# Kernel optimization log

Measured on AMD Instinct MI355X. Metric: run time of the kernel, lower is better.

## Reference

```python
import jax, jax.numpy as jnp
import numpy as np

H = 1024  # hidden_dim
D = 128   # input_dim
B = 128   # batch
S = 512   # seq_len / target_len


def _lstm_cell(inp, h, c, Wih, Whh, bih, bhh):
    # PyTorch gate order: i, f, g, o
    gates = inp @ Wih.T + h @ Whh.T + bih + bhh  # [B, 4H]
    i, f, g, o = jnp.split(gates, 4, axis=-1)
    i = jax.nn.sigmoid(i)
    f = jax.nn.sigmoid(f)
    g = jnp.tanh(g)
    o = jax.nn.sigmoid(o)
    c = f * c + i * g
    h = o * jnp.tanh(c)
    return h, c


def setup_inputs() -> dict:
    key = jax.random.key(0)
    ks = jax.random.split(key, 12)
    k = 1.0 / np.sqrt(H)  # PyTorch LSTM/Linear uniform init bound
    u = lambda kk, shp: jax.random.uniform(kk, shp, jnp.float32, -k, k)
    return {
        "x": jax.random.normal(ks[0], (B, S, D), jnp.float32),
        "enc_Wih": u(ks[1], (4 * H, D)),
        "enc_Whh": u(ks[2], (4 * H, H)),
        "enc_bih": u(ks[3], (4 * H,)),
        "enc_bhh": u(ks[4], (4 * H,)),
        "dec_Wih": u(ks[5], (4 * H, H)),
        "dec_Whh": u(ks[6], (4 * H, H)),
        "dec_bih": u(ks[7], (4 * H,)),
        "dec_bhh": u(ks[8], (4 * H,)),
        "out_W": u(ks[9], (D, H)),
        "out_b": u(ks[10], (D,)),
    }


def reference(x, enc_Wih, enc_Whh, enc_bih, enc_bhh,
              dec_Wih, dec_Whh, dec_bih, dec_bhh, out_W, out_b):
    b, s, _ = x.shape
    h0 = jnp.zeros((b, H), x.dtype)
    c0 = jnp.zeros((b, H), x.dtype)

    # ---- encoder: LSTM over time ----
    def enc_step(carry, xt):
        h, c = carry
        h, c = _lstm_cell(xt, h, c, enc_Wih, enc_Whh, enc_bih, enc_bhh)
        return (h, c), h

    (h_n, c_n), hs = jax.lax.scan(enc_step, (h0, c0), jnp.transpose(x, (1, 0, 2)))
    encoded = jnp.transpose(hs, (1, 0, 2))  # [B, S, H]

    def dec_step(carry, _):
        h, c, inp = carry
        h, c = _lstm_cell(inp, h, c, dec_Wih, dec_Whh, dec_bih, dec_bhh)
        y = h @ out_W.T + out_b  # [B, D]
        return (h, c, y), y

    init = (h_n, c_n, encoded[:, -1, :] @ jnp.eye(H, D, dtype=x.dtype) * 0 + 0)  # placeholder removed below
    # decoder_input starts as last encoder hidden (encoded_seq[:, -1:, :]) but the
    # decoder LSTM input size is H while fed-back outputs have size D in torch code;
    # torch decoder has input_size=hidden_dim, so feeding back D-dim output would
    # error in torch unless D == H. The repo uses it with the first step only having
    # H-dim input; to be runnable and faithful to the intended recurrence we pad the
    # fed-back output to H dims via the same convention torch would require: here we
    # replicate the exact torch graph, which requires feeding H-dim inputs, so we
    # project outputs back implicitly by zero-padding.
    def dec_step_pad(carry, _):
        h, c, inp = carry  # inp: [B, H]
        h, c = _lstm_cell(inp, h, c, dec_Wih, dec_Whh, dec_bih, dec_bhh)
        y = h @ out_W.T + out_b  # [B, D]
        inp_next = jnp.pad(y, ((0, 0), (0, H - D)))
        return (h, c, inp_next), y

    carry0 = (h_n, c_n, encoded[:, -1, :])
    _, ys = jax.lax.scan(dec_step_pad, carry0, None, length=s)
    recon = jnp.transpose(ys, (1, 0, 2))  # [B, S, D]

    recon_loss = jnp.mean(jnp.sum((recon - x) ** 2, axis=(1, 2)))
    return recon, encoded, recon_loss
```

## Files before the change

### kernel.cpp

```cpp
#include <hip/hip_runtime.h>


#define BB 128
#define SS 512
#define DD 128
#define HH 1024
#define G4 4096
#define KENC 1152
#define NBLK 256
#define RP 20
#define SLOTSTRIDE 16

typedef _Float16 half8 __attribute__((ext_vector_type(8)));
typedef float floatx4 __attribute__((ext_vector_type(4)));

__device__ __forceinline__ float sigf(float x) { return 1.0f / (1.0f + __expf(-x)); }
__device__ __forceinline__ float tanhfast(float x) { return 1.0f - 2.0f / (1.0f + __expf(2.0f * x)); }

#define MFMA16(a, b, c) __builtin_amdgcn_mfma_f32_16x16x32_f16((a), (b), (c), 0, 0, 0)

__device__ __forceinline__ half8 ldg_h8_sc(const _Float16* p) {
  floatx4 t;
  asm volatile("global_load_dwordx4 %0, %1, off sc0 sc1" : "=v"(t) : "v"(p) : "memory");
  return __builtin_bit_cast(half8, t);
}
__device__ __forceinline__ void stg_h_sc(_Float16* p, _Float16 v) {
  unsigned u = (unsigned)__builtin_bit_cast(unsigned short, v);
  asm volatile("global_store_short %0, %1, off sc0 sc1" :: "v"(p), "v"(u) : "memory");
}


__global__ void k_prep_encw(const float* __restrict__ eWih, const float* __restrict__ eWhh,
                            _Float16* __restrict__ encW) {
  int r = blockIdx.x;
  for (int k = threadIdx.x; k < KENC; k += blockDim.x) {
    float v = (k < DD) ? eWih[(size_t)r * DD + k] : eWhh[(size_t)r * HH + (k - DD)];
    encW[(size_t)r * KENC + k] = (_Float16)v;
  }
}

__global__ void k_prep_simple(const float* __restrict__ x, const float* __restrict__ dWih,
                              const float* __restrict__ dWhh, const float* __restrict__ oW,
                              const float* __restrict__ eBih, const float* __restrict__ eBhh,
                              const float* __restrict__ dBih, const float* __restrict__ dBhh,
                              const float* __restrict__ oB,
                              _Float16* __restrict__ x16,
                              _Float16* __restrict__ decW1, _Float16* __restrict__ outW16,
                              float* __restrict__ encB, float* __restrict__ decB1,
                              float* __restrict__ decB2,
                              _Float16* __restrict__ hA, float* __restrict__ lossAcc,
                              unsigned* __restrict__ bar) {
  int tid = blockIdx.x * blockDim.x + threadIdx.x;
  int nt = gridDim.x * blockDim.x;
  for (size_t i = tid; i < (size_t)G4 * HH; i += nt)
    decW1[i] = (_Float16)(dWih[i] + dWhh[i]);
  for (size_t i = tid; i < (size_t)BB * SS * DD; i += nt)
    x16[i] = (_Float16)x[i];
  for (size_t i = tid; i < (size_t)DD * HH; i += nt)
    outW16[i] = (_Float16)oW[i];
  for (size_t i = tid; i < (size_t)BB * HH; i += nt)
    hA[i] = (_Float16)0.0f;
  for (size_t i = tid; i < (size_t)NBLK * SLOTSTRIDE; i += nt)
    bar[i] = 0u;
  if (tid == 0) lossAcc[0] = 0.0f;
  if (tid < G4) {
    encB[tid] = eBih[tid] + eBhh[tid];
    float b1 = dBih[tid] + dBhh[tid];
    decB1[tid] = b1;
    float acc = b1;
    for (int j = 0; j < DD; ++j) acc += dWih[(size_t)tid * HH + j] * oB[j];
    decB2[tid] = acc;
  }
}

__global__ void k_prep_decw2(const float* __restrict__ dWih, const float* __restrict__ dWhh,
                             const float* __restrict__ oW, _Float16* __restrict__ decW2) {
  int r = blockIdx.x >> 2;
  int c = ((blockIdx.x & 3) << 8) + threadIdx.x;
  float acc = dWhh[(size_t)r * HH + c];
  for (int j = 0; j < DD; ++j) acc += dWih[(size_t)r * HH + j] * oW[(size_t)j * HH + c];
  decW2[(size_t)r * HH + c] = (_Float16)acc;
}

__device__ __forceinline__ void bar_arrive(unsigned* slot, unsigned step) {
  asm volatile("s_waitcnt vmcnt(0)" ::: "memory");
  __syncthreads();
  if (threadIdx.x == 0)
    __hip_atomic_store(slot, step, __ATOMIC_RELAXED, __HIP_MEMORY_SCOPE_AGENT);
}
__device__ __forceinline__ void bar_wait(unsigned* slots, int polln, unsigned step) {
  int pi = (int)threadIdx.x - (512 - polln);
  if (pi >= 0) {
    unsigned* p = slots + (size_t)pi * SLOTSTRIDE;
    while (__hip_atomic_load(p, __ATOMIC_RELAXED, __HIP_MEMORY_SCOPE_AGENT) < step)
      __builtin_amdgcn_s_sleep(4);
  }
  __syncthreads();
}


__global__ __launch_bounds__(512, 2) void k_seq(
    const float* __restrict__ x, const _Float16* __restrict__ x16,
    const _Float16* __restrict__ encW, const float* __restrict__ encB,
    const _Float16* __restrict__ decW1, const _Float16* __restrict__ decW2,
    const float* __restrict__ decB1, const float* __restrict__ decB2,
    const _Float16* __restrict__ outW, const float* __restrict__ oB,
    _Float16* __restrict__ hA, _Float16* __restrict__ hB,
    float* __restrict__ encOut, float* __restrict__ recon,
    float* __restrict__ lossAcc, float* __restrict__ lossOut,
    unsigned* __restrict__ bar) {
  __shared__ float pl[4][4][2][16][RP];
  __shared__ float red[4][2][16][RP];
  __shared__ float pY[4][2][16][RP];
  __shared__ float redY[2][16][RP];

  const int tid = threadIdx.x;
  const int lane = tid & 63, w = tid >> 6;
  const int n = lane & 15, q = lane >> 4;
  const int ut = (int)blockIdx.x & 63, mtb = (int)blockIdx.x >> 6;
  const int m0 = mtb << 5, u0 = ut << 4;
  const int kh0 = w << 7;

  const int m_l = tid >> 4, u_l = tid & 15;
  const int mtc = m_l >> 4, rowc = m_l & 15;
  const int cm = m0 + m_l, cu = u0 + u_l;
  const size_t hidx = (size_t)cm * HH + cu;

  unsigned* myslot = bar + (size_t)blockIdx.x * SLOTSTRIDE;
  unsigned* grpSlots = bar + (size_t)(mtb * 64) * SLOTSTRIDE;
  float creg = 0.0f;

  half8 bw[4][4];
  half8 xw[4];
  {
    const _Float16* base = encW + (size_t)(u0 + n) * KENC + (size_t)(DD + kh0 + q * 8);
#pragma unroll
    for (int g = 0; g < 4; ++g)
#pragma unroll
      for (int kk = 0; kk < 4; ++kk)
        bw[g][kk] = *(const half8*)(base + (size_t)g * ((size_t)HH * KENC) + kk * 32);
    if (w < 4) {
      const _Float16* xb = encW + (size_t)(u0 + n) * KENC + (size_t)((w << 5) + q * 8);
#pragma unroll
      for (int g = 0; g < 4; ++g)
        xw[g] = *(const half8*)(xb + (size_t)g * ((size_t)HH * KENC));
    }
  }
  float b0 = encB[cu], b1 = encB[HH + cu], b2 = encB[2 * HH + cu], b3 = encB[3 * HH + cu];

  const _Float16* hrowA = hA + (size_t)(m0 + n) * HH + kh0 + q * 8;
  const _Float16* hrowB = hB + (size_t)(m0 + n) * HH + kh0 + q * 8;
  const _Float16* x16r0 = x16 + (size_t)(m0 + n) * ((size_t)SS * DD) + (size_t)((w << 5) + q * 8);
  const _Float16* x16r1 = x16r0 + (size_t)16 * ((size_t)SS * DD);
  float* encPtr = encOut + (size_t)cm * ((size_t)SS * HH) + cu;

  for (int t = 0; t < SS; ++t) {
    floatx4 acc[4][2];
#pragma unroll
    for (int g = 0; g < 4; ++g) {
      acc[g][0] = (floatx4){0, 0, 0, 0};
      acc[g][1] = (floatx4){0, 0, 0, 0};
    }
    if (w < 4) {
      half8 xa0 = *(const half8*)(x16r0 + (size_t)t * DD);
      half8 xa1 = *(const half8*)(x16r1 + (size_t)t * DD);
      acc[0][0] = MFMA16(xa0, xw[0], acc[0][0]); acc[0][1] = MFMA16(xa1, xw[0], acc[0][1]);
      acc[1][0] = MFMA16(xa0, xw[1], acc[1][0]); acc[1][1] = MFMA16(xa1, xw[1], acc[1][1]);
      acc[2][0] = MFMA16(xa0, xw[2], acc[2][0]); acc[2][1] = MFMA16(xa1, xw[2], acc[2][1]);
      acc[3][0] = MFMA16(xa0, xw[3], acc[3][0]); acc[3][1] = MFMA16(xa1, xw[3], acc[3][1]);
    }
    if (t > 0) bar_wait(grpSlots, 64, (unsigned)t);

    const _Float16* h0 = (t & 1) ? hrowB : hrowA;
    const _Float16* h1 = h0 + (size_t)16 * HH;
    half8 ha[4], hb[4];
#pragma unroll
    for (int kk = 0; kk < 4; ++kk) {
      ha[kk] = ldg_h8_sc(h0 + kk * 32);
      hb[kk] = ldg_h8_sc(h1 + kk * 32);
    }
    asm volatile("s_waitcnt vmcnt(0)" ::: "memory");
    __builtin_amdgcn_sched_barrier(0);
#pragma unroll
    for (int kk = 0; kk < 4; ++kk) {
      acc[0][0] = MFMA16(ha[kk], bw[0][kk], acc[0][0]); acc[0][1] = MFMA16(hb[kk], bw[0][kk], acc[0][1]);
      acc[1][0] = MFMA16(ha[kk], bw[1][kk], acc[1][0]); acc[1][1] = MFMA16(hb[kk], bw[1][kk], acc[1][1]);
      acc[2][0] = MFMA16(ha[kk], bw[2][kk], acc[2][0]); acc[2][1] = MFMA16(hb[kk], bw[2][kk], acc[2][1]);
      acc[3][0] = MFMA16(ha[kk], bw[3][kk], acc[3][0]); acc[3][1] = MFMA16(hb[kk], bw[3][kk], acc[3][1]);
    }

    if (w >= 4) {
#pragma unroll
      for (int g = 0; g < 4; ++g)
#pragma unroll
        for (int mt = 0; mt < 2; ++mt)
#pragma unroll
          for (int r = 0; r < 4; ++r)
            pl[w - 4][g][mt][q * 4 + r][n] = acc[g][mt][r];
    }
    __syncthreads();
    if (w < 4) {
#pragma unroll
      for (int g = 0; g < 4; ++g)
#pragma unroll
        for (int mt = 0; mt < 2; ++mt)
#pragma unroll
          for (int r = 0; r < 4; ++r) {
            acc[g][mt][r] += pl[w][g][mt][q * 4 + r][n];
            pl[w][g][mt][q * 4 + r][n] = acc[g][mt][r];
          }
    }
    __syncthreads();
    {
      int base = tid * 4;
      int col = base & 15, row = (base >> 4) & 15, mt = (base >> 8) & 1, g = base >> 9;
      floatx4 s = *(const floatx4*)&pl[0][g][mt][row][col];
      s += *(const floatx4*)&pl[1][g][mt][row][col];
      s += *(const floatx4*)&pl[2][g][mt][row][col];
      s += *(const floatx4*)&pl[3][g][mt][row][col];
      *(floatx4*)&red[g][mt][row][col] = s;
    }
    __syncthreads();
    {
      float gi = sigf(red[0][mtc][rowc][u_l] + b0);
      float gf = sigf(red[1][mtc][rowc][u_l] + b1);
      float gg = tanhfast(red[2][mtc][rowc][u_l] + b2);
      float go = sigf(red[3][mtc][rowc][u_l] + b3);
      float cv = gf * creg + gi * gg;
      creg = cv;
      float hv = go * tanhfast(cv);
      stg_h_sc(((t & 1) ? hA : hB) + hidx, (_Float16)hv);
      encPtr[0] = hv;
      encPtr += HH;
    }
    bar_arrive(myslot, (unsigned)(t + 1));
  }

  {
    const _Float16* base = decW1 + (size_t)(u0 + n) * HH + (size_t)(kh0 + q * 8);
#pragma unroll
    for (int g = 0; g < 4; ++g)
#pragma unroll
      for (int kk = 0; kk < 4; ++kk)
        bw[g][kk] = *(const half8*)(base + (size_t)g * ((size_t)HH * HH) + kk * 32);
  }
  b0 = decB1[cu]; b1 = decB1[HH + cu]; b2 = decB1[2 * HH + cu]; b3 = decB1[3 * HH + cu];

  half8 ow[4];
  if (ut < 8) {
    const _Float16* oro = outW + (size_t)(u0 + n) * HH + (size_t)(kh0 + q * 8);
#pragma unroll
    for (int kk = 0; kk < 4; ++kk) ow[kk] = *(const half8*)(oro + kk * 32);
  }
  const float obv_cu = (ut < 8) ? oB[cu] : 0.0f;

  for (int s = 1; s <= SS; ++s) {
    if (s == 2) {
      const _Float16* base = decW2 + (size_t)(u0 + n) * HH + (size_t)(kh0 + q * 8);
#pragma unroll
      for (int g = 0; g < 4; ++g)
#pragma unroll
        for (int kk = 0; kk < 4; ++kk)
          bw[g][kk] = *(const half8*)(base + (size_t)g * ((size_t)HH * HH) + kk * 32);
      b0 = decB2[cu]; b1 = decB2[HH + cu]; b2 = decB2[2 * HH + cu]; b3 = decB2[3 * HH + cu];
    }
    bar_wait(grpSlots, 64, (unsigned)(511 + s));

    const int p = 511 + s;
    const _Float16* h0 = (p & 1) ? hrowB : hrowA;
    const _Float16* h1 = h0 + (size_t)16 * HH;
    const bool doY = (s >= 2) && (ut < 8);

    floatx4 acc[4][2];
#pragma unroll
    for (int g = 0; g < 4; ++g) {
      acc[g][0] = (floatx4){0, 0, 0, 0};
      acc[g][1] = (floatx4){0, 0, 0, 0};
    }
    floatx4 accY[2];
    accY[0] = (floatx4){0, 0, 0, 0}; accY[1] = (floatx4){0, 0, 0, 0};

    half8 ha[4], hb[4];
#pragma unroll
    for (int kk = 0; kk < 4; ++kk) {
      ha[kk] = ldg_h8_sc(h0 + kk * 32);
      hb[kk] = ldg_h8_sc(h1 + kk * 32);
    }
    asm volatile("s_waitcnt vmcnt(0)" ::: "memory");
    __builtin_amdgcn_sched_barrier(0);
#pragma unroll
    for (int kk = 0; kk < 4; ++kk) {
      acc[0][0] = MFMA16(ha[kk], bw[0][kk], acc[0][0]); acc[0][1] = MFMA16(hb[kk], bw[0][kk], acc[0][1]);
      acc[1][0] = MFMA16(ha[kk], bw[1][kk], acc[1][0]); acc[1][1] = MFMA16(hb[kk], bw[1][kk], acc[1][1]);
      acc[2][0] = MFMA16(ha[kk], bw[2][kk], acc[2][0]); acc[2][1] = MFMA16(hb[kk], bw[2][kk], acc[2][1]);
      acc[3][0] = MFMA16(ha[kk], bw[3][kk], acc[3][0]); acc[3][1] = MFMA16(hb[kk], bw[3][kk], acc[3][1]);
      if (doY) {
        accY[0] = MFMA16(ha[kk], ow[kk], accY[0]);
        accY[1] = MFMA16(hb[kk], ow[kk], accY[1]);
      }
    }

    if (w >= 4) {
#pragma unroll
      for (int g = 0; g < 4; ++g)
#pragma unroll
        for (int mt = 0; mt < 2; ++mt)
#pragma unroll
          for (int r = 0; r < 4; ++r)
            pl[w - 4][g][mt][q * 4 + r][n] = acc[g][mt][r];
      if (doY)
#pragma unroll
        for (int mt = 0; mt < 2; ++mt)
#pragma unroll
          for (int r = 0; r < 4; ++r)
            pY[w - 4][mt][q * 4 + r][n] = accY[mt][r];
    }
    __syncthreads();
    if (w < 4) {
#pragma unroll
      for (int g = 0; g < 4; ++g)
#pragma unroll
        for (int mt = 0; mt < 2; ++mt)
#pragma unroll
          for (int r = 0; r < 4; ++r) {
            acc[g][mt][r] += pl[w][g][mt][q * 4 + r][n];
            pl[w][g][mt][q * 4 + r][n] = acc[g][mt][r];
          }
      if (doY)
#pragma unroll
        for (int mt = 0; mt < 2; ++mt)
#pragma unroll
          for (int r = 0; r < 4; ++r) {
            accY[mt][r] += pY[w][mt][q * 4 + r][n];
            pY[w][mt][q * 4 + r][n] = accY[mt][r];
          }
    }
    __syncthreads();
    {
      int base = tid * 4;
      int col = base & 15, row = (base >> 4) & 15, mt = (base >> 8) & 1, g = base >> 9;
      floatx4 sv = *(const floatx4*)&pl[0][g][mt][row][col];
      sv += *(const floatx4*)&pl[1][g][mt][row][col];
      sv += *(const floatx4*)&pl[2][g][mt][row][col];
      sv += *(const floatx4*)&pl[3][g][mt][row][col];
      *(floatx4*)&red[g][mt][row][col] = sv;
    }
    if (doY && tid < 128) {
      int base = tid * 4;
      int col = base & 15, row = (base >> 4) & 15, mt = (base >> 8) & 1;
      floatx4 sv = *(const floatx4*)&pY[0][mt][row][col];
      sv += *(const floatx4*)&pY[1][mt][row][col];
      sv += *(const floatx4*)&pY[2][mt][row][col];
      sv += *(const floatx4*)&pY[3][mt][row][col];
      *(floatx4*)&redY[mt][row][col] = sv;
    }
    __syncthreads();
    {
      float gi = sigf(red[0][mtc][rowc][u_l] + b0);
      float gf = sigf(red[1][mtc][rowc][u_l] + b1);
      float gg = tanhfast(red[2][mtc][rowc][u_l] + b2);
      float go = sigf(red[3][mtc][rowc][u_l] + b3);
      float cv = gf * creg + gi * gg;
      creg = cv;
      float hv = go * tanhfast(cv);
      stg_h_sc(((p & 1) ? hA : hB) + hidx, (_Float16)hv);
      if (doY) {
        int ty = s - 2;
        float yv = redY[mtc][rowc][u_l] + obv_cu;
        size_t ix = (size_t)cm * ((size_t)SS * DD) + (size_t)ty * DD + cu;
        recon[ix] = yv;
        float e = yv - x[ix];
        float ls = e * e;
#pragma unroll
        for (int off = 32; off; off >>= 1) ls += __shfl_xor(ls, off, 64);
        if (lane == 0) atomicAdd(lossAcc, ls);
      }
    }
    bar_arrive(myslot, (unsigned)(512 + s));
  }

  bar_wait(bar, 256, 1024u);
  if ((int)blockIdx.x < 64 && tid < 64) {
    const int fmt = (int)blockIdx.x >> 3, fdt = (int)blockIdx.x & 7;
    const int fm0 = fmt << 4, d0 = fdt << 4;
    floatx4 a4 = (floatx4){0, 0, 0, 0};
    const _Float16* hrow = hA + (size_t)(fm0 + n) * HH + q * 8;
    const _Float16* orow = outW + (size_t)(d0 + n) * HH + q * 8;
    for (int kb = 0; kb < 32; kb += 8) {
      half8 hh[8];
#pragma unroll
      for (int j = 0; j < 8; ++j) hh[j] = ldg_h8_sc(hrow + (size_t)(kb + j) * 32);
      asm volatile("s_waitcnt vmcnt(0)" ::: "memory");
      __builtin_amdgcn_sched_barrier(0);
#pragma unroll
      for (int j = 0; j < 8; ++j)
        a4 = MFMA16(hh[j], *(const half8*)(orow + (size_t)(kb + j) * 32), a4);
    }
    int d = d0 + n;
    float ob2 = oB[d];
    float ls = 0.0f;
#pragma unroll
    for (int r = 0; r < 4; ++r) {
      int m = fm0 + q * 4 + r;
      float yv = a4[r] + ob2;
      size_t ix = (size_t)m * ((size_t)SS * DD) + (size_t)(SS - 1) * DD + d;
      recon[ix] = yv;
      float e = yv - x[ix];
      ls += e * e;
    }
#pragma unroll
    for (int off = 32; off; off >>= 1) ls += __shfl_xor(ls, off, 64);
    if (lane == 0) atomicAdd(lossAcc, ls);
  }
  bar_arrive(myslot, 1025u);
  bar_wait(bar, 256, 1025u);
  if (blockIdx.x == 0 && tid == 0)
    lossOut[0] = __hip_atomic_load(lossAcc, __ATOMIC_RELAXED, __HIP_MEMORY_SCOPE_AGENT) *
                 (1.0f / (float)BB);
}


extern "C" void kernel_launch(void* const* d_in, const int* in_sizes, int n_in,
                              void* d_out, int out_size, void* d_ws, size_t ws_size,
                              hipStream_t stream) {
  const float* x    = (const float*)d_in[0];
  const float* eWih = (const float*)d_in[1];
  const float* eWhh = (const float*)d_in[2];
  const float* eBih = (const float*)d_in[3];
  const float* eBhh = (const float*)d_in[4];
  const float* dWih = (const float*)d_in[5];
  const float* dWhh = (const float*)d_in[6];
  const float* dBih = (const float*)d_in[7];
  const float* dBhh = (const float*)d_in[8];
  const float* oW   = (const float*)d_in[9];
  const float* oB   = (const float*)d_in[10];

  float* out = (float*)d_out;
  float* recon = out;
  float* encOut = out + (size_t)BB * SS * DD;
  float* lossOut = out + (size_t)BB * SS * DD + (size_t)BB * SS * HH;

  char* p = (char*)d_ws;
  auto alloc = [&](size_t bytes) {
    char* r = p;
    p += (bytes + 255) & ~(size_t)255;
    return r;
  };
  _Float16* encW   = (_Float16*)alloc((size_t)G4 * KENC * 2);
  _Float16* decW1  = (_Float16*)alloc((size_t)G4 * HH * 2);
  _Float16* decW2  = (_Float16*)alloc((size_t)G4 * HH * 2);
  _Float16* outW16 = (_Float16*)alloc((size_t)DD * HH * 2);
  _Float16* x16    = (_Float16*)alloc((size_t)BB * SS * DD * 2);
  float* encB  = (float*)alloc((size_t)G4 * 4);
  float* decB1 = (float*)alloc((size_t)G4 * 4);
  float* decB2 = (float*)alloc((size_t)G4 * 4);
  _Float16* hA = (_Float16*)alloc((size_t)BB * HH * 2);
  _Float16* hB = (_Float16*)alloc((size_t)BB * HH * 2);
  float* lossAcc = (float*)alloc(256);
  unsigned* bar = (unsigned*)alloc((size_t)NBLK * SLOTSTRIDE * 4);
  (void)in_sizes; (void)n_in; (void)out_size; (void)ws_size;

  k_prep_encw<<<G4, 256, 0, stream>>>(eWih, eWhh, encW);
  k_prep_simple<<<2048, 256, 0, stream>>>(x, dWih, dWhh, oW, eBih, eBhh, dBih, dBhh, oB,
                                          x16, decW1, outW16, encB, decB1, decB2, hA,
                                          lossAcc, bar);
  k_prep_decw2<<<G4 * 4, 256, 0, stream>>>(dWih, dWhh, oW, decW2);

  void* args[] = {(void*)&x, (void*)&x16, (void*)&encW, (void*)&encB, (void*)&decW1,
                  (void*)&decW2, (void*)&decB1, (void*)&decB2, (void*)&outW16, (void*)&oB,
                  (void*)&hA, (void*)&hB, (void*)&encOut, (void*)&recon,
                  (void*)&lossAcc, (void*)&lossOut, (void*)&bar};
  (void)hipLaunchCooperativeKernel((void*)k_seq, dim3(NBLK), dim3(512), args, 0, stream);
}
```

Baseline: 6.137 ms.

## Split K per wave with per-wave producer polling and single-pass reduction

Waves are reassigned so each handles one 16-row batch tile and a 256-wide K slice, instead of two row tiles and a 128-wide slice. Each wave now polls only the 16 producer blocks that own its K slice, rather than the whole block waiting on all 64. The two-stage shared-memory reduction with three barriers becomes a single barrier and a direct four-way sum. Loss partials are kept in registers and flushed with one atomic per block at the end, and the poll sleep is shortened. The cost is twice as many weight registers per wave, and the output-projection weights are now reloaded from global memory every step.

New measurement: 5.704 ms. 7.1% less time.

```diff
diff --git a/kernel.cpp b/kernel.cpp
--- a/kernel.cpp
+++ b/kernel.cpp
@@ -82,18 +82,27 @@
   decW2[(size_t)r * HH + c] = (_Float16)acc;
 }
 
-__device__ __forceinline__ void bar_arrive(unsigned* slot, unsigned step) {
+
+__device__ __forceinline__ void block_arrive(unsigned* slot, unsigned step) {
   asm volatile("s_waitcnt vmcnt(0)" ::: "memory");
   __syncthreads();
   if (threadIdx.x == 0)
     __hip_atomic_store(slot, step, __ATOMIC_RELAXED, __HIP_MEMORY_SCOPE_AGENT);
 }
-__device__ __forceinline__ void bar_wait(unsigned* slots, int polln, unsigned step) {
-  int pi = (int)threadIdx.x - (512 - polln);
-  if (pi >= 0) {
-    unsigned* p = slots + (size_t)pi * SLOTSTRIDE;
+__device__ __forceinline__ void wave_wait16(unsigned* slots, unsigned step) {
+  int l = (int)threadIdx.x & 63;
+  if (l < 16) {
+    unsigned* p = slots + (size_t)l * SLOTSTRIDE;
     while (__hip_atomic_load(p, __ATOMIC_RELAXED, __HIP_MEMORY_SCOPE_AGENT) < step)
-      __builtin_amdgcn_s_sleep(4);
+      __builtin_amdgcn_s_sleep(2);
+  }
+}
+__device__ __forceinline__ void bar_wait_all(unsigned* bar, unsigned step) {
+  int pi = (int)threadIdx.x;
+  if (pi < NBLK) {
+    unsigned* p = bar + (size_t)pi * SLOTSTRIDE;
+    while (__hip_atomic_load(p, __ATOMIC_RELAXED, __HIP_MEMORY_SCOPE_AGENT) < step)
+      __builtin_amdgcn_s_sleep(2);
   }
   __syncthreads();
 }
@@ -110,122 +119,88 @@
     float* __restrict__ lossAcc, float* __restrict__ lossOut,
     unsigned* __restrict__ bar) {
   __shared__ float pl[4][4][2][16][RP];
-  __shared__ float red[4][2][16][RP];
   __shared__ float pY[4][2][16][RP];
-  __shared__ float redY[2][16][RP];
+  __shared__ float lred[8];
 
   const int tid = threadIdx.x;
   const int lane = tid & 63, w = tid >> 6;
   const int n = lane & 15, q = lane >> 4;
+  const int mtw = w >> 2, ksl = w & 3;
   const int ut = (int)blockIdx.x & 63, mtb = (int)blockIdx.x >> 6;
   const int m0 = mtb << 5, u0 = ut << 4;
-  const int kh0 = w << 7;
 
   const int m_l = tid >> 4, u_l = tid & 15;
   const int mtc = m_l >> 4, rowc = m_l & 15;
   const int cm = m0 + m_l, cu = u0 + u_l;
   const size_t hidx = (size_t)cm * HH + cu;
 
+  const floatx4 zero4 = {0.0f, 0.0f, 0.0f, 0.0f};
+
   unsigned* myslot = bar + (size_t)blockIdx.x * SLOTSTRIDE;
-  unsigned* grpSlots = bar + (size_t)(mtb * 64) * SLOTSTRIDE;
+  unsigned* prodSlots = bar + (size_t)(mtb * 64 + ksl * 16) * SLOTSTRIDE;
   float creg = 0.0f;
-
-  half8 bw[4][4];
+  float lossReg = 0.0f;
+
+  half8 bw[4][8];
   half8 xw[4];
   {
-    const _Float16* base = encW + (size_t)(u0 + n) * KENC + (size_t)(DD + kh0 + q * 8);
-#pragma unroll
-    for (int g = 0; g < 4; ++g)
-#pragma unroll
-      for (int kk = 0; kk < 4; ++kk)
+    const _Float16* base = encW + (size_t)(u0 + n) * KENC + (size_t)(DD + ksl * 256 + q * 8);
+    const _Float16* xb   = encW + (size_t)(u0 + n) * KENC + (size_t)(ksl * 32 + q * 8);
+#pragma unroll
+    for (int g = 0; g < 4; ++g) {
+#pragma unroll
+      for (int kk = 0; kk < 8; ++kk)
         bw[g][kk] = *(const half8*)(base + (size_t)g * ((size_t)HH * KENC) + kk * 32);
-    if (w < 4) {
-      const _Float16* xb = encW + (size_t)(u0 + n) * KENC + (size_t)((w << 5) + q * 8);
-#pragma unroll
-      for (int g = 0; g < 4; ++g)
-        xw[g] = *(const half8*)(xb + (size_t)g * ((size_t)HH * KENC));
+      xw[g] = *(const half8*)(xb + (size_t)g * ((size_t)HH * KENC));
     }
   }
   float b0 = encB[cu], b1 = encB[HH + cu], b2 = encB[2 * HH + cu], b3 = encB[3 * HH + cu];
 
-  const _Float16* hrowA = hA + (size_t)(m0 + n) * HH + kh0 + q * 8;
-  const _Float16* hrowB = hB + (size_t)(m0 + n) * HH + kh0 + q * 8;
-  const _Float16* x16r0 = x16 + (size_t)(m0 + n) * ((size_t)SS * DD) + (size_t)((w << 5) + q * 8);
-  const _Float16* x16r1 = x16r0 + (size_t)16 * ((size_t)SS * DD);
+  const _Float16* hTA = hA + (size_t)(m0 + mtw * 16 + n) * HH + ksl * 256 + q * 8;
+  const _Float16* hTB = hB + (size_t)(m0 + mtw * 16 + n) * HH + ksl * 256 + q * 8;
+  const _Float16* xp = x16 + (size_t)(m0 + mtw * 16 + n) * ((size_t)SS * DD) + ksl * 32 + q * 8;
   float* encPtr = encOut + (size_t)cm * ((size_t)SS * HH) + cu;
 
   for (int t = 0; t < SS; ++t) {
-    floatx4 acc[4][2];
-#pragma unroll
-    for (int g = 0; g < 4; ++g) {
-      acc[g][0] = (floatx4){0, 0, 0, 0};
-      acc[g][1] = (floatx4){0, 0, 0, 0};
-    }
-    if (w < 4) {
-      half8 xa0 = *(const half8*)(x16r0 + (size_t)t * DD);
-      half8 xa1 = *(const half8*)(x16r1 + (size_t)t * DD);
-      acc[0][0] = MFMA16(xa0, xw[0], acc[0][0]); acc[0][1] = MFMA16(xa1, xw[0], acc[0][1]);
-      acc[1][0] = MFMA16(xa0, xw[1], acc[1][0]); acc[1][1] = MFMA16(xa1, xw[1], acc[1][1]);
-      acc[2][0] = MFMA16(xa0, xw[2], acc[2][0]); acc[2][1] = MFMA16(xa1, xw[2], acc[2][1]);
-      acc[3][0] = MFMA16(xa0, xw[3], acc[3][0]); acc[3][1] = MFMA16(xa1, xw[3], acc[3][1]);
-    }
-    if (t > 0) bar_wait(grpSlots, 64, (unsigned)t);
-
-    const _Float16* h0 = (t & 1) ? hrowB : hrowA;
-    const _Float16* h1 = h0 + (size_t)16 * HH;
-    half8 ha[4], hb[4];
-#pragma unroll
-    for (int kk = 0; kk < 4; ++kk) {
-      ha[kk] = ldg_h8_sc(h0 + kk * 32);
-      hb[kk] = ldg_h8_sc(h1 + kk * 32);
-    }
+    half8 xa = *(const half8*)(xp + (size_t)t * DD);
+    if (t > 0) wave_wait16(prodSlots, (unsigned)t);
+
+    const _Float16* hsrc = (t & 1) ? hTB : hTA;
+    half8 ha[8];
+#pragma unroll
+    for (int kk = 0; kk < 8; ++kk) ha[kk] = ldg_h8_sc(hsrc + kk * 32);
     asm volatile("s_waitcnt vmcnt(0)" ::: "memory");
     __builtin_amdgcn_sched_barrier(0);
-#pragma unroll
-    for (int kk = 0; kk < 4; ++kk) {
-      acc[0][0] = MFMA16(ha[kk], bw[0][kk], acc[0][0]); acc[0][1] = MFMA16(hb[kk], bw[0][kk], acc[0][1]);
-      acc[1][0] = MFMA16(ha[kk], bw[1][kk], acc[1][0]); acc[1][1] = MFMA16(hb[kk], bw[1][kk], acc[1][1]);
-      acc[2][0] = MFMA16(ha[kk], bw[2][kk], acc[2][0]); acc[2][1] = MFMA16(hb[kk], bw[2][kk], acc[2][1]);
-      acc[3][0] = MFMA16(ha[kk], bw[3][kk], acc[3][0]); acc[3][1] = MFMA16(hb[kk], bw[3][kk], acc[3][1]);
-    }
-
-    if (w >= 4) {
+
+    floatx4 acc[4];
+#pragma unroll
+    for (int g = 0; g < 4; ++g) acc[g] = MFMA16(xa, xw[g], zero4);
+#pragma unroll
+    for (int kk = 0; kk < 8; ++kk)
 #pragma unroll
       for (int g = 0; g < 4; ++g)
-#pragma unroll
-        for (int mt = 0; mt < 2; ++mt)
-#pragma unroll
-          for (int r = 0; r < 4; ++r)
-            pl[w - 4][g][mt][q * 4 + r][n] = acc[g][mt][r];
-    }
+        acc[g] = MFMA16(ha[kk], bw[g][kk], acc[g]);
+
+#pragma unroll
+    for (int g = 0; g < 4; ++g)
+#pragma unroll
+      for (int r = 0; r < 4; ++r)
+        pl[ksl][g][mtw][q * 4 + r][n] = acc[g][r];
     __syncthreads();
-    if (w < 4) {
-#pragma unroll
-      for (int g = 0; g < 4; ++g)
-#pragma unroll
-        for (int mt = 0; mt < 2; ++mt)
-#pragma unroll
-          for (int r = 0; r < 4; ++r) {
-            acc[g][mt][r] += pl[w][g][mt][q * 4 + r][n];
-            pl[w][g][mt][q * 4 + r][n] = acc[g][mt][r];
-          }
-    }
-    __syncthreads();
+
     {
-      int base = tid * 4;
-      int col = base & 15, row = (base >> 4) & 15, mt = (base >> 8) & 1, g = base >> 9;
-      floatx4 s = *(const floatx4*)&pl[0][g][mt][row][col];
-      s += *(const floatx4*)&pl[1][g][mt][row][col];
-      s += *(const floatx4*)&pl[2][g][mt][row][col];
-      s += *(const floatx4*)&pl[3][g][mt][row][col];
-      *(floatx4*)&red[g][mt][row][col] = s;
-    }
-    __syncthreads();
-    {
-      float gi = sigf(red[0][mtc][rowc][u_l] + b0);
-      float gf = sigf(red[1][mtc][rowc][u_l] + b1);
-      float gg = tanhfast(red[2][mtc][rowc][u_l] + b2);
-      float go = sigf(red[3][mtc][rowc][u_l] + b3);
+      float s0 = pl[0][0][mtc][rowc][u_l] + pl[1][0][mtc][rowc][u_l] +
+                 pl[2][0][mtc][rowc][u_l] + pl[3][0][mtc][rowc][u_l];
+      float s1 = pl[0][1][mtc][rowc][u_l] + pl[1][1][mtc][rowc][u_l] +
+                 pl[2][1][mtc][rowc][u_l] + pl[3][1][mtc][rowc][u_l];
+      float s2 = pl[0][2][mtc][rowc][u_l] + pl[1][2][mtc][rowc][u_l] +
+                 pl[2][2][mtc][rowc][u_l] + pl[3][2][mtc][rowc][u_l];
+      float s3 = pl[0][3][mtc][rowc][u_l] + pl[1][3][mtc][rowc][u_l] +
+                 pl[2][3][mtc][rowc][u_l] + pl[3][3][mtc][rowc][u_l];
+      float gi = sigf(s0 + b0);
+      float gf = sigf(s1 + b1);
+      float gg = tanhfast(s2 + b2);
+      float go = sigf(s3 + b3);
       float cv = gf * creg + gi * gg;
       creg = cv;
       float hv = go * tanhfast(cv);
@@ -233,157 +208,103 @@
       encPtr[0] = hv;
       encPtr += HH;
     }
-    bar_arrive(myslot, (unsigned)(t + 1));
+    block_arrive(myslot, (unsigned)(t + 1));
   }
 
   {
-    const _Float16* base = decW1 + (size_t)(u0 + n) * HH + (size_t)(kh0 + q * 8);
+    const _Float16* base = decW1 + (size_t)(u0 + n) * HH + (size_t)(ksl * 256 + q * 8);
 #pragma unroll
     for (int g = 0; g < 4; ++g)
 #pragma unroll
-      for (int kk = 0; kk < 4; ++kk)
+      for (int kk = 0; kk < 8; ++kk)
         bw[g][kk] = *(const half8*)(base + (size_t)g * ((size_t)HH * HH) + kk * 32);
   }
   b0 = decB1[cu]; b1 = decB1[HH + cu]; b2 = decB1[2 * HH + cu]; b3 = decB1[3 * HH + cu];
 
-  half8 ow[4];
-  if (ut < 8) {
-    const _Float16* oro = outW + (size_t)(u0 + n) * HH + (size_t)(kh0 + q * 8);
-#pragma unroll
-    for (int kk = 0; kk < 4; ++kk) ow[kk] = *(const half8*)(oro + kk * 32);
-  }
-  const float obv_cu = (ut < 8) ? oB[cu] : 0.0f;
+  const bool isY = (ut < 8);
+  const _Float16* owp = outW + (size_t)(u0 + n) * HH + ksl * 256 + q * 8;
+  const float obv_cu = isY ? oB[cu] : 0.0f;
 
   for (int s = 1; s <= SS; ++s) {
     if (s == 2) {
-      const _Float16* base = decW2 + (size_t)(u0 + n) * HH + (size_t)(kh0 + q * 8);
+      const _Float16* base = decW2 + (size_t)(u0 + n) * HH + (size_t)(ksl * 256 + q * 8);
 #pragma unroll
       for (int g = 0; g < 4; ++g)
 #pragma unroll
-        for (int kk = 0; kk < 4; ++kk)
+        for (int kk = 0; kk < 8; ++kk)
           bw[g][kk] = *(const half8*)(base + (size_t)g * ((size_t)HH * HH) + kk * 32);
       b0 = decB2[cu]; b1 = decB2[HH + cu]; b2 = decB2[2 * HH + cu]; b3 = decB2[3 * HH + cu];
     }
-    bar_wait(grpSlots, 64, (unsigned)(511 + s));
-
     const int p = 511 + s;
-    const _Float16* h0 = (p & 1) ? hrowB : hrowA;
-    const _Float16* h1 = h0 + (size_t)16 * HH;
-    const bool doY = (s >= 2) && (ut < 8);
-
-    floatx4 acc[4][2];
-#pragma unroll
-    for (int g = 0; g < 4; ++g) {
-      acc[g][0] = (floatx4){0, 0, 0, 0};
-      acc[g][1] = (floatx4){0, 0, 0, 0};
-    }
-    floatx4 accY[2];
-    accY[0] = (floatx4){0, 0, 0, 0}; accY[1] = (floatx4){0, 0, 0, 0};
-
-    half8 ha[4], hb[4];
-#pragma unroll
-    for (int kk = 0; kk < 4; ++kk) {
-      ha[kk] = ldg_h8_sc(h0 + kk * 32);
-      hb[kk] = ldg_h8_sc(h1 + kk * 32);
-    }
+    const bool doY = (s >= 2) && isY;
+
+    wave_wait16(prodSlots, (unsigned)p);
+
+    const _Float16* hsrc = (p & 1) ? hTB : hTA;
+    half8 ha[8];
+#pragma unroll
+    for (int kk = 0; kk < 8; ++kk) ha[kk] = ldg_h8_sc(hsrc + kk * 32);
     asm volatile("s_waitcnt vmcnt(0)" ::: "memory");
     __builtin_amdgcn_sched_barrier(0);
-#pragma unroll
-    for (int kk = 0; kk < 4; ++kk) {
-      acc[0][0] = MFMA16(ha[kk], bw[0][kk], acc[0][0]); acc[0][1] = MFMA16(hb[kk], bw[0][kk], acc[0][1]);
-      acc[1][0] = MFMA16(ha[kk], bw[1][kk], acc[1][0]); acc[1][1] = MFMA16(hb[kk], bw[1][kk], acc[1][1]);
-      acc[2][0] = MFMA16(ha[kk], bw[2][kk], acc[2][0]); acc[2][1] = MFMA16(hb[kk], bw[2][kk], acc[2][1]);
-      acc[3][0] = MFMA16(ha[kk], bw[3][kk], acc[3][0]); acc[3][1] = MFMA16(hb[kk], bw[3][kk], acc[3][1]);
-      if (doY) {
-        accY[0] = MFMA16(ha[kk], ow[kk], accY[0]);
-        accY[1] = MFMA16(hb[kk], ow[kk], accY[1]);
-      }
-    }
-
-    if (w >= 4) {
+
+    floatx4 acc[4];
+#pragma unroll
+    for (int g = 0; g < 4; ++g) acc[g] = zero4;
+    floatx4 accY = zero4;
+#pragma unroll
+    for (int kk = 0; kk < 8; ++kk) {
 #pragma unroll
       for (int g = 0; g < 4; ++g)
-#pragma unroll
-        for (int mt = 0; mt < 2; ++mt)
-#pragma unroll
-          for (int r = 0; r < 4; ++r)
-            pl[w - 4][g][mt][q * 4 + r][n] = acc[g][mt][r];
-      if (doY)
-#pragma unroll
-        for (int mt = 0; mt < 2; ++mt)
-#pragma unroll
-          for (int r = 0; r < 4; ++r)
-            pY[w - 4][mt][q * 4 + r][n] = accY[mt][r];
-    }
+        acc[g] = MFMA16(ha[kk], bw[g][kk], acc[g]);
+      if (doY) accY = MFMA16(ha[kk], *(const half8*)(owp + kk * 32), accY);
+    }
+
+#pragma unroll
+    for (int g = 0; g < 4; ++g)
+#pragma unroll
+      for (int r = 0; r < 4; ++r)
+        pl[ksl][g][mtw][q * 4 + r][n] = acc[g][r];
+    if (doY)
+#pragma unroll
+      for (int r = 0; r < 4; ++r)
+        pY[ksl][mtw][q * 4 + r][n] = accY[r];
     __syncthreads();
-    if (w < 4) {
-#pragma unroll
-      for (int g = 0; g < 4; ++g)
-#pragma unroll
-        for (int mt = 0; mt < 2; ++mt)
-#pragma unroll
-          for (int r = 0; r < 4; ++r) {
-            acc[g][mt][r] += pl[w][g][mt][q * 4 + r][n];
-            pl[w][g][mt][q * 4 + r][n] = acc[g][mt][r];
-          }
-      if (doY)
-#pragma unroll
-        for (int mt = 0; mt < 2; ++mt)
-#pragma unroll
-          for (int r = 0; r < 4; ++r) {
-            accY[mt][r] += pY[w][mt][q * 4 + r][n];
-            pY[w][mt][q * 4 + r][n] = accY[mt][r];
-          }
-    }
-    __syncthreads();
+
     {
-      int base = tid * 4;
-      int col = base & 15, row = (base >> 4) & 15, mt = (base >> 8) & 1, g = base >> 9;
-      floatx4 sv = *(const floatx4*)&pl[0][g][mt][row][col];
-      sv += *(const floatx4*)&pl[1][g][mt][row][col];
-      sv += *(const floatx4*)&pl[2][g][mt][row][col];
-      sv += *(const floatx4*)&pl[3][g][mt][row][col];
-      *(floatx4*)&red[g][mt][row][col] = sv;
-    }
-    if (doY && tid < 128) {
-      int base = tid * 4;
-      int col = base & 15, row = (base >> 4) & 15, mt = (base >> 8) & 1;
-      floatx4 sv = *(const floatx4*)&pY[0][mt][row][col];
-      sv += *(const floatx4*)&pY[1][mt][row][col];
-      sv += *(const floatx4*)&pY[2][mt][row][col];
-      sv += *(const floatx4*)&pY[3][mt][row][col];
-      *(floatx4*)&redY[mt][row][col] = sv;
-    }
-    __syncthreads();
-    {
-      float gi = sigf(red[0][mtc][rowc][u_l] + b0);
-      float gf = sigf(red[1][mtc][rowc][u_l] + b1);
-      float gg = tanhfast(red[2][mtc][rowc][u_l] + b2);
-      float go = sigf(red[3][mtc][rowc][u_l] + b3);
+      float s0 = pl[0][0][mtc][rowc][u_l] + pl[1][0][mtc][rowc][u_l] +
+                 pl[2][0][mtc][rowc][u_l] + pl[3][0][mtc][rowc][u_l];
+      float s1 = pl[0][1][mtc][rowc][u_l] + pl[1][1][mtc][rowc][u_l] +
+                 pl[2][1][mtc][rowc][u_l] + pl[3][1][mtc][rowc][u_l];
+      float s2 = pl[0][2][mtc][rowc][u_l] + pl[1][2][mtc][rowc][u_l] +
+                 pl[2][2][mtc][rowc][u_l] + pl[3][2][mtc][rowc][u_l];
+      float s3 = pl[0][3][mtc][rowc][u_l] + pl[1][3][mtc][rowc][u_l] +
+                 pl[2][3][mtc][rowc][u_l] + pl[3][3][mtc][rowc][u_l];
+      float gi = sigf(s0 + b0);
+      float gf = sigf(s1 + b1);
+      float gg = tanhfast(s2 + b2);
+      float go = sigf(s3 + b3);
       float cv = gf * creg + gi * gg;
       creg = cv;
       float hv = go * tanhfast(cv);
       stg_h_sc(((p & 1) ? hA : hB) + hidx, (_Float16)hv);
       if (doY) {
         int ty = s - 2;
-        float yv = redY[mtc][rowc][u_l] + obv_cu;
+        float yv = pY[0][mtc][rowc][u_l] + pY[1][mtc][rowc][u_l] +
+                   pY[2][mtc][rowc][u_l] + pY[3][mtc][rowc][u_l] + obv_cu;
         size_t ix = (size_t)cm * ((size_t)SS * DD) + (size_t)ty * DD + cu;
         recon[ix] = yv;
         float e = yv - x[ix];
-        float ls = e * e;
-#pragma unroll
-        for (int off = 32; off; off >>= 1) ls += __shfl_xor(ls, off, 64);
-        if (lane == 0) atomicAdd(lossAcc, ls);
+        lossReg += e * e;
       }
     }
-    bar_arrive(myslot, (unsigned)(512 + s));
-  }
-
-  bar_wait(bar, 256, 1024u);
+    block_arrive(myslot, (unsigned)(p + 1));
+  }
+
+  bar_wait_all(bar, 1024u);
   if ((int)blockIdx.x < 64 && tid < 64) {
     const int fmt = (int)blockIdx.x >> 3, fdt = (int)blockIdx.x & 7;
     const int fm0 = fmt << 4, d0 = fdt << 4;
-    floatx4 a4 = (floatx4){0, 0, 0, 0};
+    floatx4 a4 = zero4;
     const _Float16* hrow = hA + (size_t)(fm0 + n) * HH + q * 8;
     const _Float16* orow = outW + (size_t)(d0 + n) * HH + q * 8;
     for (int kb = 0; kb < 32; kb += 8) {
@@ -398,7 +319,6 @@
     }
     int d = d0 + n;
     float ob2 = oB[d];
-    float ls = 0.0f;
 #pragma unroll
     for (int r = 0; r < 4; ++r) {
       int m = fm0 + q * 4 + r;
@@ -406,14 +326,22 @@
       size_t ix = (size_t)m * ((size_t)SS * DD) + (size_t)(SS - 1) * DD + d;
       recon[ix] = yv;
       float e = yv - x[ix];
-      ls += e * e;
-    }
-#pragma unroll
-    for (int off = 32; off; off >>= 1) ls += __shfl_xor(ls, off, 64);
-    if (lane == 0) atomicAdd(lossAcc, ls);
-  }
-  bar_arrive(myslot, 1025u);
-  bar_wait(bar, 256, 1025u);
+      lossReg += e * e;
+    }
+  }
+
+#pragma unroll
+  for (int off = 32; off; off >>= 1) lossReg += __shfl_xor(lossReg, off, 64);
+  if (lane == 0) lred[w] = lossReg;
+  __syncthreads();
+  if (tid == 0) {
+    float t = 0.0f;
+#pragma unroll
+    for (int i = 0; i < 8; ++i) t += lred[i];
+    if (t != 0.0f) atomicAdd(lossAcc, t);
+  }
+  block_arrive(myslot, 1025u);
+  bar_wait_all(bar, 1025u);
   if (blockIdx.x == 0 && tid == 0)
     lossOut[0] = __hip_atomic_load(lossAcc, __ATOMIC_RELAXED, __HIP_MEMORY_SCOPE_AGENT) *
                  (1.0f / (float)BB);
```
